# Performance work log

Measured on AMD Instinct MI355X. Metric: run time of the kernel, lower is better.

Reference implementation:

```python
import jax, jax.numpy as jnp
import numpy as np
from jax import lax

B, T_DEC, T_ENC = 32, 400, 300
N_MEL, PRENET, ENC_D = 80, 256, 512
ATT_RNN, DEC_RNN, ATT_D = 512, 512, 128
LOC_F, LOC_K = 32, 31


def setup_inputs() -> dict:
    key = jax.random.key(0)
    ks = jax.random.split(key, 24)

    def w(k, shape):
        return jax.random.normal(k, shape, jnp.float32) / np.float32(np.sqrt(shape[-1]))

    inp = {
        "encoder_out": jax.random.normal(ks[0], (B, T_ENC, ENC_D), jnp.float32),
        "mels": jax.random.normal(ks[1], (B, T_DEC, N_MEL), jnp.float32),
        "lengths": jax.random.randint(ks[2], (B,), 1, T_ENC + 1).astype(jnp.int32),
        # prenet (3 layers, no bias)
        "W_p0": w(ks[3], (PRENET, N_MEL)),
        "W_p1": w(ks[4], (PRENET, PRENET)),
        "W_p2": w(ks[5], (PRENET, PRENET)),
        # attention GRUCell: input = prenet_dim + enc_dim = 768
        "W_ih_a": w(ks[6], (3 * ATT_RNN, PRENET + ENC_D)),
        "W_hh_a": w(ks[7], (3 * ATT_RNN, ATT_RNN)),
        "b_ih_a": jnp.zeros((3 * ATT_RNN,), jnp.float32),
        "b_hh_a": jnp.zeros((3 * ATT_RNN,), jnp.float32),
        # decoder GRUCell: input = attn_rnn + enc_dim = 1024 (what the code actually feeds)
        "W_ih_d": w(ks[8], (3 * DEC_RNN, ATT_RNN + ENC_D)),
        "W_hh_d": w(ks[9], (3 * DEC_RNN, DEC_RNN)),
        "b_ih_d": jnp.zeros((3 * DEC_RNN,), jnp.float32),
        "b_hh_d": jnp.zeros((3 * DEC_RNN,), jnp.float32),
        # location-sensitive attention
        "W_q": w(ks[10], (ATT_D, ATT_RNN)),
        "W_m": w(ks[11], (ATT_D, ENC_D)),
        "K_loc": w(ks[12], (LOC_F, 2, LOC_K)),
        "W_l": w(ks[13], (ATT_D, LOC_F)),
        "v": w(ks[14], (ATT_D,)),
        # output projection + gate
        "W_out": w(ks[15], (N_MEL, DEC_RNN + ENC_D)),
        "b_out": jnp.zeros((N_MEL,), jnp.float32),
        "W_g": w(ks[16], (1, DEC_RNN + ENC_D)),
        "b_g": jnp.zeros((1,), jnp.float32),
    }
    return inp


def _gru_cell(x, h, W_ih, W_hh, b_ih, b_hh):
    gi = x @ W_ih.T + b_ih
    gh = h @ W_hh.T + b_hh
    i_r, i_z, i_n = jnp.split(gi, 3, axis=-1)
    h_r, h_z, h_n = jnp.split(gh, 3, axis=-1)
    r = jax.nn.sigmoid(i_r + h_r)
    z = jax.nn.sigmoid(i_z + h_z)
    n = jnp.tanh(i_n + r * h_n)
    return (1.0 - z) * n + z * h


def _decoder_core(encoder_out, mels, lengths, W_p0, W_p1, W_p2,
                  W_ih_a, W_hh_a, b_ih_a, b_hh_a, W_ih_d, W_hh_d, b_ih_d, b_hh_d,
                  W_q, W_m, K_loc, W_l, v, W_out, b_out, W_g, b_g):
    Bb, T_enc, _ = encoder_out.shape
    T_dec = mels.shape[1]
    pmem = encoder_out @ W_m.T  # [B,T_enc,ATT_D], computed once
    enc_mask = jnp.arange(T_enc)[None, :] < lengths[:, None]  # [B,T_enc]
    # shifted teacher-forcing inputs: zero first frame, then mels[:, :-1]
    dec_inputs = jnp.concatenate(
        [jnp.zeros((Bb, 1, mels.shape[2]), mels.dtype), mels[:, :-1]], axis=1)
    drop_key = jax.random.key(42)
    pad = LOC_K // 2

    def prenet(x, t):
        for i, W in enumerate((W_p0, W_p1, W_p2)):
            x = jax.nn.relu(x @ W.T)
            k = jax.random.fold_in(drop_key, t * 3 + i)
            keep = jax.random.bernoulli(k, 0.5, x.shape)
            x = jnp.where(keep, x * 2.0, 0.0)  # inverted dropout p=0.5 (hardcoded training=True)
        return x

    def step(carry, xs):
        ah, dh, ctx, aw, aw_sum = carry
        frame, t = xs
        x = prenet(frame, t)
        ah = _gru_cell(jnp.concatenate([x, ctx], -1), ah, W_ih_a, W_hh_a, b_ih_a, b_hh_a)
        # location features from current + cumulative attention weights
        awc = jnp.stack([aw, aw_sum], axis=1)  # [B,2,T_enc]
        loc = lax.conv_general_dilated(awc, K_loc, (1,), [(pad, pad)],
                                       dimension_numbers=("NCH", "OIH", "NCH"))
        loc = jnp.swapaxes(loc, 1, 2) @ W_l.T  # [B,T_enc,ATT_D]
        e = jnp.tanh((ah @ W_q.T)[:, None, :] + pmem + loc) @ v  # [B,T_enc]
        e = jnp.where(enc_mask, e, -1e9)
        aw_new = jax.nn.softmax(e, axis=-1)
        ctx = jnp.einsum("bt,btd->bd", aw_new, encoder_out)
        aw_sum = aw_sum + aw_new
        dh = _gru_cell(jnp.concatenate([ah, ctx], -1), dh, W_ih_d, W_hh_d, b_ih_d, b_hh_d)
        dhc = jnp.concatenate([dh, ctx], -1)
        mel = dhc @ W_out.T + b_out  # [B,N_MEL]
        gate = (dhc @ W_g.T + b_g)[:, 0]  # [B]
        return (ah, dh, ctx, aw_new, aw_sum), (mel, gate, aw_new)

    f32 = encoder_out.dtype
    init = (jnp.zeros((Bb, ATT_RNN), f32), jnp.zeros((Bb, DEC_RNN), f32),
            jnp.zeros((Bb, ENC_D), f32), jnp.zeros((Bb, T_enc), f32),
            jnp.zeros((Bb, T_enc), f32))
    frames = jnp.swapaxes(dec_inputs, 0, 1)  # [T_dec,B,N_MEL]
    _, (mels_out, gates, aligns) = lax.scan(jax.checkpoint(step), init,
                                            (frames, jnp.arange(T_dec)))
    mel_outputs = jnp.transpose(mels_out, (1, 2, 0))  # [B,N_MEL,T_dec]
    gate_outputs = jnp.swapaxes(gates, 0, 1)          # [B,T_dec]
    alignments = jnp.swapaxes(aligns, 0, 1)           # [B,T_dec,T_enc]
    return mel_outputs, gate_outputs, alignments


def reference(encoder_out, mels, lengths, W_p0, W_p1, W_p2,
              W_ih_a, W_hh_a, b_ih_a, b_hh_a, W_ih_d, W_hh_d, b_ih_d, b_hh_d,
              W_q, W_m, K_loc, W_l, v, W_out, b_out, W_g, b_g):
    return _decoder_core(encoder_out, mels, lengths, W_p0, W_p1, W_p2,
                         W_ih_a, W_hh_a, b_ih_a, b_hh_a, W_ih_d, W_hh_d, b_ih_d, b_hh_d,
                         W_q, W_m, K_loc, W_l, v, W_out, b_out, W_g, b_g)
```

## Files before the change

### kernel.cpp

```cpp
#include <hip/hip_runtime.h>
#include <cstdint>


static constexpr int TDEC = 400, TENC = 300, NMEL = 80;

__device__ __forceinline__ uint2 threefry2x32(uint32_t k0, uint32_t k1,
                                              uint32_t x0, uint32_t x1) {
  uint32_t k2 = k0 ^ k1 ^ 0x1BD11BDAu;
  x0 += k0; x1 += k1;
#define TFR(r) { x0 += x1; x1 = (x1 << (r)) | (x1 >> (32 - (r))); x1 ^= x0; }
  TFR(13) TFR(15) TFR(26) TFR(6)
  x0 += k1; x1 += k2 + 1u;
  TFR(17) TFR(29) TFR(16) TFR(24)
  x0 += k2; x1 += k0 + 2u;
  TFR(13) TFR(15) TFR(26) TFR(6)
  x0 += k0; x1 += k1 + 3u;
  TFR(17) TFR(29) TFR(16) TFR(24)
  x0 += k1; x1 += k2 + 4u;
  TFR(13) TFR(15) TFR(26) TFR(6)
  x0 += k2; x1 += k0 + 5u;
#undef TFR
  return make_uint2(x0, x1);
}

__device__ __forceinline__ bool keep_mask(uint32_t key0, uint32_t key1, uint32_t idx) {
  uint2 o = threefry2x32(key0, key1, 0u, idx);
  uint32_t bits = o.x ^ o.y;
  float u = __uint_as_float((bits >> 9) | 0x3f800000u) - 1.0f;
  return u < 0.5f;
}

__device__ __forceinline__ float dot4(float4 w, float4 a) {
  return w.x * a.x + w.y * a.y + w.z * a.z + w.w * a.w;
}
__device__ __forceinline__ float nt_load(const float* p) {
  return __builtin_nontemporal_load(p);
}

__device__ __forceinline__ void s_rel(float* p, float v) {
  __hip_atomic_store(p, v, __ATOMIC_RELAXED, __HIP_MEMORY_SCOPE_AGENT);
}
__device__ __forceinline__ float l_rel(const float* p) {
  return __hip_atomic_load(p, __ATOMIC_RELAXED, __HIP_MEMORY_SCOPE_AGENT);
}
__device__ __forceinline__ float4 l4(const float4* p) {
  const unsigned long long* q = (const unsigned long long*)p;
  unsigned long long a = __hip_atomic_load(q, __ATOMIC_RELAXED, __HIP_MEMORY_SCOPE_AGENT);
  unsigned long long b = __hip_atomic_load(q + 1, __ATOMIC_RELAXED, __HIP_MEMORY_SCOPE_AGENT);
  float4 r;
  ((unsigned long long*)&r)[0] = a;
  ((unsigned long long*)&r)[1] = b;
  return r;
}

__device__ __forceinline__ void gsync(int* arrive, int* release, int bno) {
  __syncthreads();
  if (blockIdx.x == 0) {
    if (threadIdx.x > 0)
      while (__hip_atomic_load(&arrive[threadIdx.x * 32], __ATOMIC_RELAXED,
                               __HIP_MEMORY_SCOPE_AGENT) < bno)
        __builtin_amdgcn_s_sleep(16);
    __syncthreads();
    if (threadIdx.x < 8)
      __hip_atomic_store(&release[threadIdx.x * 32], bno, __ATOMIC_RELEASE,
                         __HIP_MEMORY_SCOPE_AGENT);
  } else {
    if (threadIdx.x == 0) {
      __hip_atomic_store(&arrive[blockIdx.x * 32], bno, __ATOMIC_RELEASE,
                         __HIP_MEMORY_SCOPE_AGENT);
      while (__hip_atomic_load(&release[(blockIdx.x & 7) * 32], __ATOMIC_RELAXED,
                               __HIP_MEMORY_SCOPE_AGENT) < bno)
        __builtin_amdgcn_s_sleep(16);
    }
  }
  __syncthreads();
}

template <int K>
__device__ __forceinline__ void prenet_layer(const float* in_lds, float* out_lds,
                                             float* out_g, const float* __restrict__ W,
                                             uint32_t key0, uint32_t key1, int b0) {
  const int tid = threadIdx.x;
  const int cgp = tid & 63, bg = tid >> 6;
  float acc[4][4];
#pragma unroll
  for (int cc = 0; cc < 4; ++cc)
#pragma unroll
    for (int rr = 0; rr < 4; ++rr) acc[cc][rr] = 0.f;
  const float4* W4 = (const float4*)W;
  const float4* in4 = (const float4*)in_lds;
  for (int k4 = 0; k4 < K / 4; ++k4) {
    float4 a[4];
#pragma unroll
    for (int rr = 0; rr < 4; ++rr) a[rr] = in4[(bg * 4 + rr) * (K / 4) + k4];
#pragma unroll
    for (int cc = 0; cc < 4; ++cc) {
      float4 w = W4[(cgp + 64 * cc) * (K / 4) + k4];
#pragma unroll
      for (int rr = 0; rr < 4; ++rr) acc[cc][rr] += dot4(w, a[rr]);
    }
  }
#pragma unroll
  for (int cc = 0; cc < 4; ++cc)
#pragma unroll
    for (int rr = 0; rr < 4; ++rr) {
      int c = cgp + 64 * cc, br = bg * 4 + rr;
      float val = fmaxf(acc[cc][rr], 0.f);
      val = keep_mask(key0, key1, (uint32_t)((b0 + br) * 256 + c)) ? val * 2.f : 0.f;
      if (out_lds) out_lds[br * 256 + c] = val;
      if (out_g) out_g[(b0 + br) * 256 + c] = val;
    }
  __syncthreads();
}

__global__ __launch_bounds__(256) void prenet_kernel(const float* __restrict__ mels,
                                                     const float* __restrict__ Wp0,
                                                     const float* __restrict__ Wp1,
                                                     const float* __restrict__ Wp2,
                                                     float* __restrict__ x_all) {
  __shared__ float bufA[16 * 256];
  __shared__ float bufB[16 * 256];
  const int t = blockIdx.x >> 1, b0 = (blockIdx.x & 1) * 16;
  const int tid = threadIdx.x;
  for (int i = tid; i < 16 * 80; i += 256) {
    int br = i / 80, k = i % 80;
    bufB[br * 80 + k] = (t == 0) ? 0.f : mels[((b0 + br) * TDEC + (t - 1)) * NMEL + k];
  }
  __syncthreads();
  uint2 k0v = threefry2x32(0u, 42u, 0u, (uint32_t)(t * 3 + 0));
  uint2 k1v = threefry2x32(0u, 42u, 0u, (uint32_t)(t * 3 + 1));
  uint2 k2v = threefry2x32(0u, 42u, 0u, (uint32_t)(t * 3 + 2));
  prenet_layer<80>(bufB, bufA, nullptr, Wp0, k0v.x, k0v.y, b0);
  prenet_layer<256>(bufA, bufB, nullptr, Wp1, k1v.x, k1v.y, b0);
  prenet_layer<256>(bufB, nullptr, x_all + t * 8192, Wp2, k2v.x, k2v.y, b0);
}

__global__ __launch_bounds__(256) void pmem_kernel(const float* __restrict__ enc,
                                                   const float* __restrict__ Wm,
                                                   float* __restrict__ pmem) {
  const int b = blockIdx.x / 10, pc = blockIdx.x % 10;
  const int j = threadIdx.x & 127, ph = threadIdx.x >> 7;
  const float4* Wm4 = (const float4*)Wm;
  const float4* enc4 = (const float4*)enc + (size_t)(b * 300 + pc * 30 + ph * 15) * 128;
  float acc[15];
#pragma unroll
  for (int pp = 0; pp < 15; ++pp) acc[pp] = 0.f;
  for (int k4 = 0; k4 < 128; ++k4) {
    float4 w = Wm4[j * 128 + k4];
#pragma unroll
    for (int pp = 0; pp < 15; ++pp) acc[pp] += dot4(w, enc4[pp * 128 + k4]);
  }
#pragma unroll
  for (int pp = 0; pp < 15; ++pp)
    pmem[(size_t)(b * 300 + pc * 30 + ph * 15 + pp) * 128 + j] = acc[pp];
}

struct DP {
  const float *xall, *enc, *pmem;
  const int* lens;
  const float *Wiha, *Whha, *biha, *bhha;
  const float *Wihd, *Whhd, *bihd, *bhhd;
  const float *Wq, *Kloc, *Wl, *vv, *Wout, *bout, *Wg, *bg;
  float *ah, *dh, *ctxM;
  float *e2;
  float *pM, *pS;
  float *V;
  float *awsum2;
  int *arrive, *release, *rM;
  float *omel, *ogate, *oalign;
};

__global__ __launch_bounds__(256, 1) void decoder_kernel(DP P) {
  __shared__ float4 pinW[4608];
  __shared__ float scr[6144];
  __shared__ float2 tapsL[992];
  const int tid = threadIdx.x, blk = blockIdx.x;
  const int er = blk >> 2, eq = blk & 3, pb = eq * 75;

  if (blk < 128) {
    const float4* Wih4 = (const float4*)P.Wiha;
    const float4* Whh4 = (const float4*)P.Whha;
    int idx0 = blk * 4;
    for (int i = tid; i < 2304; i += 256) {
      int g = i / 768, rem = i % 768, r2 = rem / 192, k4 = rem % 192;
      pinW[i] = Wih4[(size_t)(g * 512 + idx0 + r2) * 192 + k4];
    }
    for (int i = tid; i < 1536; i += 256) {
      int g = i / 512, rem = i % 512, r2 = rem / 128, k4 = rem % 128;
      pinW[2304 + i] = Whh4[(size_t)(g * 512 + idx0 + r2) * 128 + k4];
    }
  } else {
    const float4* Wih4 = (const float4*)P.Wihd;
    const float4* Whh4 = (const float4*)P.Whhd;
    int idx0 = (blk - 128) * 4;
    for (int i = tid; i < 3072; i += 256) {
      int g = i / 1024, rem = i % 1024, r2 = rem / 256, k4 = rem % 256;
      pinW[i] = Wih4[(size_t)(g * 512 + idx0 + r2) * 256 + k4];
    }
    for (int i = tid; i < 1536; i += 256) {
      int g = i / 512, rem = i % 512, r2 = rem / 128, k4 = rem % 128;
      pinW[3072 + i] = Whh4[(size_t)(g * 512 + idx0 + r2) * 128 + k4];
    }
  }
  for (int i = tid; i < 992; i += 256) {
    int f = i / 31, k = i % 31;
    tapsL[i] = make_float2(P.Kloc[f * 62 + k], P.Kloc[f * 62 + 31 + k]);
  }
  __syncthreads();

  int bno = 0;
  for (int t = 0; t <= TDEC; ++t) {
    const int p0 = t & 1, p1 = p0 ^ 1;

    {
      const bool isAtt = (blk < 128);
      const bool act = isAtt ? (t < TDEC) : (t >= 1);
      if (act) {
        const int row = tid >> 3, seg = tid & 7;
        const int idx0 = (isAtt ? blk : (blk - 128)) * 4;
        const int K4I = isAtt ? 192 : 256;
        const int SI = K4I / 8, a4n = isAtt ? 64 : 128;
        const float4* WihL = pinW;
        const float4* WhhL = pinW + (isAtt ? 2304 : 3072);
        const float4* A4p = isAtt ? (const float4*)(P.xall + (size_t)t * 8192) : nullptr;
        const float4* Ab = isAtt ? nullptr : (const float4*)(P.ah + p1 * 16384);
        const float4* C4 = (const float4*)(P.ctxM + p1 * 16384);
        const float4* H4 = isAtt ? (const float4*)(P.ah + p1 * 16384)
                                 : (const float4*)(P.dh + p0 * 16384);
        const float* bih = isAtt ? P.biha : P.bihd;
        const float* bhh = isAtt ? P.bhha : P.bhhd;
        const float* hpv = isAtt ? (P.ah + p1 * 16384) : (P.dh + p0 * 16384);
        float* hout = isAtt ? (P.ah + p0 * 16384) : (P.dh + p1 * 16384);

        float acc[24];
#pragma unroll
        for (int g = 0; g < 24; ++g) acc[g] = 0.f;
        for (int sb = 0; sb < SI; sb += 8) {
          float4 av[8];
#pragma unroll
          for (int u = 0; u < 8; ++u) {
            int k4 = (sb + u) * 8 + seg;
            if (k4 < a4n) av[u] = isAtt ? A4p[row * a4n + k4] : l4(&Ab[row * a4n + k4]);
            else av[u] = l4(&C4[row * 128 + (k4 - a4n)]);
          }
#pragma unroll
          for (int u = 0; u < 8; ++u) {
            int k4 = (sb + u) * 8 + seg;
#pragma unroll
            for (int g = 0; g < 3; ++g)
#pragma unroll
              for (int i = 0; i < 4; ++i)
                acc[g * 4 + i] += dot4(WihL[(g * 4 + i) * K4I + k4], av[u]);
          }
        }
        for (int sb = 0; sb < 16; sb += 8) {
          float4 hv[8];
#pragma unroll
          for (int u = 0; u < 8; ++u) {
            int k4 = (sb + u) * 8 + seg;
            hv[u] = l4(&H4[row * 128 + k4]);
          }
#pragma unroll
          for (int u = 0; u < 8; ++u) {
            int k4 = (sb + u) * 8 + seg;
#pragma unroll
            for (int g = 0; g < 3; ++g)
#pragma unroll
              for (int i = 0; i < 4; ++i)
                acc[12 + g * 4 + i] += dot4(WhhL[(g * 4 + i) * 128 + k4], hv[u]);
          }
        }
#pragma unroll
        for (int g = 0; g < 24; ++g) scr[(g * 32 + row) * 8 + seg] = acc[g];
        __syncthreads();
        if (tid < 128) {
          int i = tid >> 5, r = tid & 31;
          float gi[3], gh[3];
#pragma unroll
          for (int g = 0; g < 3; ++g) {
            float si = 0.f, sh = 0.f;
#pragma unroll
            for (int s = 0; s < 8; ++s) {
              si += scr[((g * 4 + i) * 32 + r) * 8 + s];
              sh += scr[((12 + g * 4 + i) * 32 + r) * 8 + s];
            }
            gi[g] = si + bih[g * 512 + idx0 + i];
            gh[g] = sh + bhh[g * 512 + idx0 + i];
          }
          float rr = 1.f / (1.f + expf(-(gi[0] + gh[0])));
          float zz = 1.f / (1.f + expf(-(gi[1] + gh[1])));
          float nn = tanhf(gi[2] + rr * gh[2]);
          float hp = l_rel(&hpv[r * 512 + idx0 + i]);
          s_rel(&hout[r * 512 + idx0 + i], (1.f - zz) * nn + zz * hp);
        }
      }
    }
    gsync(P.arrive, P.release, ++bno);

    if (blk < 128) {
      float* awW = scr;
      float* asW = scr + 105;
      float* convl = scr + 216;
      float* qp = scr + 2688;
      float* qb = scr + 2944;
      float* el = scr + 3072;
      float* eex = scr + 3152;
      float* ahS = scr + 3232;

      if (t < TDEC) {
        float v0s = l_rel(&P.ah[p0 * 16384 + er * 512 + tid]);
        float v1s = l_rel(&P.ah[p0 * 16384 + er * 512 + 256 + tid]);
        ahS[tid] = v0s;
        ahS[256 + tid] = v1s;
      }

      if (t >= 1) {
        float pMv[4], pSv[4];
#pragma unroll
        for (int j = 0; j < 4; ++j) pMv[j] = l_rel(&P.pM[p1 * 128 + er * 4 + j]);
#pragma unroll
        for (int j = 0; j < 4; ++j) pSv[j] = l_rel(&P.pS[p1 * 128 + er * 4 + j]);
        float M = fmaxf(fmaxf(pMv[0], pMv[1]), fmaxf(pMv[2], pMv[3]));
        float Z = 0.f;
#pragma unroll
        for (int j = 0; j < 4; ++j) Z += pSv[j] * expf(pMv[j] - M);
        float inv = 1.f / Z;
        for (int i = tid; i < 105; i += 256) {
          int p = pb - 15 + i;
          float a = 0.f, s = 0.f;
          if (p >= 0 && p < TENC) {
            float ev = l_rel(&P.e2[p1 * 9728 + er * 304 + p]);
            float sv = l_rel(&P.awsum2[p1 * 9600 + er * 300 + p]);
            a = expf(ev - M) * inv;
            s = sv + a;
          }
          awW[i] = a;
          asW[i] = s;
          if (p >= pb && p < pb + 75) {
            s_rel(&P.awsum2[p0 * 9600 + er * 300 + p], s);
            P.oalign[((size_t)(er * 400 + (t - 1))) * 300 + p] = a;
          }
        }
      } else {
        for (int i = tid; i < 105; i += 256) { awW[i] = 0.f; asW[i] = 0.f; }
      }
      __syncthreads();

      if (t < TDEC) {
        {
          int f = tid & 31, pl0 = tid >> 5;
          for (int pl = pl0; pl < 75; pl += 8) {
            float a = 0.f;
#pragma unroll
            for (int k = 0; k < 31; ++k) {
              float2 tv = tapsL[f * 31 + k];
              a += awW[pl + k] * tv.x + asW[pl + k] * tv.y;
            }
            convl[f * 77 + pl] = a;
          }
        }
        {
          int j = tid & 127, kh = tid >> 7;
          const float4* Wq4 = (const float4*)P.Wq;
          const float4* a4 = (const float4*)ahS;
          float acc = 0.f;
          for (int k4 = kh * 64; k4 < kh * 64 + 64; ++k4)
            acc += dot4(Wq4[j * 128 + k4], a4[k4]);
          qp[j * 2 + kh] = acc;
        }
        __syncthreads();
        if (tid < 128) qb[tid] = qp[tid * 2] + qp[tid * 2 + 1];
        __syncthreads();
        {
          int w = tid >> 6, lane = tid & 63;
          float wl0[32], wl1[32];
#pragma unroll
          for (int f = 0; f < 32; ++f) {
            wl0[f] = P.Wl[lane * 32 + f];
            wl1[f] = P.Wl[(lane + 64) * 32 + f];
          }
          float v0 = P.vv[lane], v1 = P.vv[lane + 64];
          float q0 = qb[lane], q1 = qb[64 + lane];
          int len = P.lens[er];
          for (int pl = w; pl < 75; pl += 4) {
            int p = pb + pl;
            float a0 = 0.f, a1 = 0.f;
#pragma unroll
            for (int f = 0; f < 32; ++f) {
              float c = convl[f * 77 + pl];
              a0 += c * wl0[f];
              a1 += c * wl1[f];
            }
            float e0 = tanhf(q0 + P.pmem[((size_t)er * 300 + p) * 128 + lane] + a0) * v0;
            float e1 = tanhf(q1 + P.pmem[((size_t)er * 300 + p) * 128 + 64 + lane] + a1) * v1;
            float es = e0 + e1;
#pragma unroll
            for (int off = 32; off > 0; off >>= 1) es += __shfl_xor(es, off, 64);
            if (lane == 0) {
              float ev = (p < len) ? es : -1e9f;
              s_rel(&P.e2[p0 * 9728 + er * 304 + p], ev);
              el[pl] = ev;
            }
          }
        }
        __syncthreads();
        if (tid < 64) {
          int lane = tid;
          float m = -3.4e38f;
          for (int i = lane; i < 75; i += 64) m = fmaxf(m, el[i]);
#pragma unroll
          for (int off = 32; off > 0; off >>= 1) m = fmaxf(m, __shfl_xor(m, off, 64));
          float s = 0.f;
          for (int i = lane; i < 75; i += 64) {
            float x = expf(el[i] - m);
            eex[i] = x;
            s += x;
          }
#pragma unroll
          for (int off = 32; off > 0; off >>= 1) s += __shfl_xor(s, off, 64);
          if (lane == 0) {
            s_rel(&P.pM[p0 * 128 + er * 4 + eq], m);
            s_rel(&P.pS[p0 * 128 + er * 4 + eq], s);
          }
        }
        __syncthreads();
        {
          float* Vw = P.V + (size_t)p0 * 65536 + (size_t)(er * 4 + eq) * 512;
#pragma unroll
          for (int cc = 0; cc < 2; ++cc) {
            int c = tid + cc * 256;
            float acc = 0.f;
            const float* eb = P.enc + ((size_t)(er * 300 + pb)) * 512 + c;
            for (int po = 0; po < 75; ++po) acc += eex[po] * nt_load(eb + (size_t)po * 512);
            s_rel(&Vw[c], acc);
          }
        }
        __syncthreads();
        if (tid == 0)
          __hip_atomic_store(&P.rM[(er * 4 + eq) * 32], t + 1, __ATOMIC_RELEASE,
                             __HIP_MEMORY_SCOPE_AGENT);
        if (eq == 0) {
          if (tid < 3)
            while (__hip_atomic_load(&P.rM[(er * 4 + 1 + tid) * 32], __ATOMIC_RELAXED,
                                     __HIP_MEMORY_SCOPE_AGENT) < t + 1)
              __builtin_amdgcn_s_sleep(8);
          __syncthreads();
          float pMv[4], pSv[4];
#pragma unroll
          for (int j = 0; j < 4; ++j) pMv[j] = l_rel(&P.pM[p0 * 128 + er * 4 + j]);
#pragma unroll
          for (int j = 0; j < 4; ++j) pSv[j] = l_rel(&P.pS[p0 * 128 + er * 4 + j]);
          float M = fmaxf(fmaxf(pMv[0], pMv[1]), fmaxf(pMv[2], pMv[3]));
          float Z = 0.f, wq[4];
#pragma unroll
          for (int j = 0; j < 4; ++j) {
            wq[j] = expf(pMv[j] - M);
            Z += pSv[j] * wq[j];
          }
          float invZ = 1.f / Z;
          const float* Vb = P.V + (size_t)p0 * 65536 + (size_t)(er * 4) * 512;
#pragma unroll
          for (int cc = 0; cc < 2; ++cc) {
            int c = tid + cc * 256;
            float vv4[4];
#pragma unroll
            for (int j = 0; j < 4; ++j) vv4[j] = l_rel(&Vb[j * 512 + c]);
            float acc = vv4[0] * wq[0] + vv4[1] * wq[1] + vv4[2] * wq[2] + vv4[3] * wq[3];
            s_rel(&P.ctxM[p0 * 16384 + er * 512 + c], acc * invZ);
          }
        }
      }
    } else if (blk < 160) {
      if (t >= 1) {
        const int r = blk - 128;
        float* dhcx = scr;
        float* opl = scr + 1024;
        for (int i = tid; i < 512; i += 256) {
          float d0 = l_rel(&P.dh[p1 * 16384 + r * 512 + i]);
          float c0 = l_rel(&P.ctxM[p1 * 16384 + r * 512 + i]);
          dhcx[i] = d0;
          dhcx[512 + i] = c0;
        }
        __syncthreads();
        if (tid < 162) {
          int m = tid >> 1, h = tid & 1;
          const float4* W4 = (m < 80) ? ((const float4*)P.Wout + (size_t)m * 256)
                                      : (const float4*)P.Wg;
          const float4* x4 = (const float4*)dhcx;
          float a = 0.f;
          for (int k4 = h * 128; k4 < h * 128 + 128; ++k4) a += dot4(W4[k4], x4[k4]);
          opl[tid] = a;
        }
        __syncthreads();
        if (tid < 81) {
          float sum = opl[tid * 2] + opl[tid * 2 + 1];
          if (tid < 80) P.omel[(size_t)(r * 80 + tid) * 400 + (t - 1)] = sum + P.bout[tid];
          else P.ogate[r * 400 + (t - 1)] = sum + P.bg[0];
        }
      }
    }
    gsync(P.arrive, P.release, ++bno);
  }
}

extern "C" void kernel_launch(void* const* d_in, const int* in_sizes, int n_in,
                              void* d_out, int out_size, void* d_ws, size_t ws_size,
                              hipStream_t stream) {
  const float* enc = (const float*)d_in[0];
  const float* mels = (const float*)d_in[1];
  const int* lens = (const int*)d_in[2];

  float* ws = (float*)d_ws;
  float* x_all = ws;
  float* pmem = x_all + 3276800;
  float* ah = pmem + 1228800;
  float* dh = ah + 32768;
  float* ctxM = dh + 32768;
  float* e2 = ctxM + 32768;
  float* pM = e2 + 19456;
  float* pS = pM + 256;
  float* V = pS + 256;
  float* awsum2 = V + 131072;
  int* arrive = (int*)(awsum2 + 19200);
  int* release = arrive + 8192;
  int* rM = release + 256;

  (void)hipMemsetAsync(ah, 0, (3 * 32768) * sizeof(float), stream);
  (void)hipMemsetAsync(awsum2, 0, 19200 * sizeof(float), stream);
  (void)hipMemsetAsync(arrive, 0, (8192 + 256 + 4096) * sizeof(int), stream);

  prenet_kernel<<<800, 256, 0, stream>>>(mels, (const float*)d_in[3],
                                         (const float*)d_in[4], (const float*)d_in[5],
                                         x_all);
  pmem_kernel<<<320, 256, 0, stream>>>(enc, (const float*)d_in[15], pmem);

  float* omel = (float*)d_out;
  float* ogate = omel + 32 * 80 * 400;
  float* oalign = ogate + 32 * 400;

  DP P;
  P.xall = x_all; P.enc = enc; P.pmem = pmem; P.lens = lens;
  P.Wiha = (const float*)d_in[6]; P.Whha = (const float*)d_in[7];
  P.biha = (const float*)d_in[8]; P.bhha = (const float*)d_in[9];
  P.Wihd = (const float*)d_in[10]; P.Whhd = (const float*)d_in[11];
  P.bihd = (const float*)d_in[12]; P.bhhd = (const float*)d_in[13];
  P.Wq = (const float*)d_in[14]; P.Kloc = (const float*)d_in[16];
  P.Wl = (const float*)d_in[17]; P.vv = (const float*)d_in[18];
  P.Wout = (const float*)d_in[19]; P.bout = (const float*)d_in[20];
  P.Wg = (const float*)d_in[21]; P.bg = (const float*)d_in[22];
  P.ah = ah; P.dh = dh; P.ctxM = ctxM; P.e2 = e2; P.pM = pM; P.pS = pS; P.V = V;
  P.awsum2 = awsum2;
  P.arrive = arrive; P.release = release; P.rM = rM;
  P.omel = omel; P.ogate = ogate; P.oalign = oalign;

  decoder_kernel<<<256, 256, 0, stream>>>(P);
}
```

Before: 48.70 ms.

## Decouple attention and decoder block groups with ring buffers and separate barriers

Splits the persistent kernel into two independently synchronized groups: attention blocks run their own per-step barriers and publish step progress, while decoder GRU and output blocks lag behind via an 8-deep ring buffer of attention hidden state and context. This replaces the single grid-wide barrier per step with group-local barriers, so the decoder chain can overlap with later attention steps. It also caches the processed-memory slice in LDS instead of reading it from global memory each step. The trade-offs are more workspace, flow-control spin waits, and extra LDS use.

```diff
diff --git a/kernel.cpp b/kernel.cpp
--- a/kernel.cpp
+++ b/kernel.cpp
@@ -3,6 +3,7 @@
 
 
 static constexpr int TDEC = 400, TENC = 300, NMEL = 80;
+static constexpr int RING = 8;
 
 __device__ __forceinline__ uint2 threefry2x32(uint32_t k0, uint32_t k1,
                                               uint32_t x0, uint32_t x1) {
@@ -43,6 +44,9 @@
 __device__ __forceinline__ float l_rel(const float* p) {
   return __hip_atomic_load(p, __ATOMIC_RELAXED, __HIP_MEMORY_SCOPE_AGENT);
 }
+__device__ __forceinline__ int li_rel(const int* p) {
+  return __hip_atomic_load(p, __ATOMIC_RELAXED, __HIP_MEMORY_SCOPE_AGENT);
+}
 __device__ __forceinline__ float4 l4(const float4* p) {
   const unsigned long long* q = (const unsigned long long*)p;
   unsigned long long a = __hip_atomic_load(q, __ATOMIC_RELAXED, __HIP_MEMORY_SCOPE_AGENT);
@@ -53,24 +57,24 @@
   return r;
 }
 
-__device__ __forceinline__ void gsync(int* arrive, int* release, int bno) {
+__device__ __forceinline__ void gsyncN(int* arrive, int* release, int id, int bno) {
   __syncthreads();
-  if (blockIdx.x == 0) {
-    if (threadIdx.x > 0)
+  if (id == 0) {
+    if (threadIdx.x > 0 && threadIdx.x < 128)
       while (__hip_atomic_load(&arrive[threadIdx.x * 32], __ATOMIC_RELAXED,
                                __HIP_MEMORY_SCOPE_AGENT) < bno)
-        __builtin_amdgcn_s_sleep(16);
+        __builtin_amdgcn_s_sleep(8);
     __syncthreads();
     if (threadIdx.x < 8)
       __hip_atomic_store(&release[threadIdx.x * 32], bno, __ATOMIC_RELEASE,
                          __HIP_MEMORY_SCOPE_AGENT);
   } else {
     if (threadIdx.x == 0) {
-      __hip_atomic_store(&arrive[blockIdx.x * 32], bno, __ATOMIC_RELEASE,
+      __hip_atomic_store(&arrive[id * 32], bno, __ATOMIC_RELEASE,
                          __HIP_MEMORY_SCOPE_AGENT);
-      while (__hip_atomic_load(&release[(blockIdx.x & 7) * 32], __ATOMIC_RELAXED,
+      while (__hip_atomic_load(&release[(id & 7) * 32], __ATOMIC_RELAXED,
                                __HIP_MEMORY_SCOPE_AGENT) < bno)
-        __builtin_amdgcn_s_sleep(16);
+        __builtin_amdgcn_s_sleep(8);
     }
   }
   __syncthreads();
@@ -161,12 +165,13 @@
   const float *Wiha, *Whha, *biha, *bhha;
   const float *Wihd, *Whhd, *bihd, *bhhd;
   const float *Wq, *Kloc, *Wl, *vv, *Wout, *bout, *Wg, *bg;
-  float *ah, *dh, *ctxM;
+  float *ah, *ctxM;
+  float *dh;
   float *e2;
   float *pM, *pS;
   float *V;
   float *awsum2;
-  int *arrive, *release, *rM;
+  int *arrA, *relA, *arrD, *relD, *rM, *attT, *decT;
   float *omel, *ogate, *oalign;
 };
 
@@ -174,74 +179,60 @@
   __shared__ float4 pinW[4608];
   __shared__ float scr[6144];
   __shared__ float2 tapsL[992];
+  __shared__ float pmemL[9600];
   const int tid = threadIdx.x, blk = blockIdx.x;
-  const int er = blk >> 2, eq = blk & 3, pb = eq * 75;
 
   if (blk < 128) {
-    const float4* Wih4 = (const float4*)P.Wiha;
-    const float4* Whh4 = (const float4*)P.Whha;
-    int idx0 = blk * 4;
-    for (int i = tid; i < 2304; i += 256) {
-      int g = i / 768, rem = i % 768, r2 = rem / 192, k4 = rem % 192;
-      pinW[i] = Wih4[(size_t)(g * 512 + idx0 + r2) * 192 + k4];
+    const int er = blk >> 2, eq = blk & 3, pb = eq * 75;
+    const int idx0 = blk * 4;
+    {
+      const float4* Wih4 = (const float4*)P.Wiha;
+      const float4* Whh4 = (const float4*)P.Whha;
+      for (int i = tid; i < 2304; i += 256) {
+        int g = i / 768, rem = i % 768, r2 = rem / 192, k4 = rem % 192;
+        pinW[i] = Wih4[(size_t)(g * 512 + idx0 + r2) * 192 + k4];
+      }
+      for (int i = tid; i < 1536; i += 256) {
+        int g = i / 512, rem = i % 512, r2 = rem / 128, k4 = rem % 128;
+        pinW[2304 + i] = Whh4[(size_t)(g * 512 + idx0 + r2) * 128 + k4];
+      }
+      for (int i = tid; i < 992; i += 256) {
+        int f = i / 31, k = i % 31;
+        tapsL[i] = make_float2(P.Kloc[f * 62 + k], P.Kloc[f * 62 + 31 + k]);
+      }
+      for (int i = tid; i < 9600; i += 256) {
+        int pl = i >> 7, c = i & 127;
+        pmemL[pl * 128 + c] = P.pmem[((size_t)(er * 300 + pb + pl)) * 128 + c];
+      }
     }
-    for (int i = tid; i < 1536; i += 256) {
-      int g = i / 512, rem = i % 512, r2 = rem / 128, k4 = rem % 128;
-      pinW[2304 + i] = Whh4[(size_t)(g * 512 + idx0 + r2) * 128 + k4];
-    }
-  } else {
-    const float4* Wih4 = (const float4*)P.Wihd;
-    const float4* Whh4 = (const float4*)P.Whhd;
-    int idx0 = (blk - 128) * 4;
-    for (int i = tid; i < 3072; i += 256) {
-      int g = i / 1024, rem = i % 1024, r2 = rem / 256, k4 = rem % 256;
-      pinW[i] = Wih4[(size_t)(g * 512 + idx0 + r2) * 256 + k4];
-    }
-    for (int i = tid; i < 1536; i += 256) {
-      int g = i / 512, rem = i % 512, r2 = rem / 128, k4 = rem % 128;
-      pinW[3072 + i] = Whh4[(size_t)(g * 512 + idx0 + r2) * 128 + k4];
-    }
-  }
-  for (int i = tid; i < 992; i += 256) {
-    int f = i / 31, k = i % 31;
-    tapsL[i] = make_float2(P.Kloc[f * 62 + k], P.Kloc[f * 62 + 31 + k]);
-  }
-  __syncthreads();
-
-  int bno = 0;
-  for (int t = 0; t <= TDEC; ++t) {
-    const int p0 = t & 1, p1 = p0 ^ 1;
-
-    {
-      const bool isAtt = (blk < 128);
-      const bool act = isAtt ? (t < TDEC) : (t >= 1);
-      if (act) {
+    __syncthreads();
+
+    int bno = 0;
+    for (int t = 0; t <= TDEC; ++t) {
+      const int p0 = t & 1, p1 = p0 ^ 1;
+      const int sc = t & (RING - 1), sp = (t - 1) & (RING - 1);
+      float* ahC = P.ah + sc * 16384;
+      const float* ahP = P.ah + sp * 16384;
+      const float* ctxP = P.ctxM + sp * 16384;
+
+      if (tid == 0)
+        while (li_rel(P.decT) < t - 7) __builtin_amdgcn_s_sleep(16);
+      __syncthreads();
+
+      if (t < TDEC) {
         const int row = tid >> 3, seg = tid & 7;
-        const int idx0 = (isAtt ? blk : (blk - 128)) * 4;
-        const int K4I = isAtt ? 192 : 256;
-        const int SI = K4I / 8, a4n = isAtt ? 64 : 128;
-        const float4* WihL = pinW;
-        const float4* WhhL = pinW + (isAtt ? 2304 : 3072);
-        const float4* A4p = isAtt ? (const float4*)(P.xall + (size_t)t * 8192) : nullptr;
-        const float4* Ab = isAtt ? nullptr : (const float4*)(P.ah + p1 * 16384);
-        const float4* C4 = (const float4*)(P.ctxM + p1 * 16384);
-        const float4* H4 = isAtt ? (const float4*)(P.ah + p1 * 16384)
-                                 : (const float4*)(P.dh + p0 * 16384);
-        const float* bih = isAtt ? P.biha : P.bihd;
-        const float* bhh = isAtt ? P.bhha : P.bhhd;
-        const float* hpv = isAtt ? (P.ah + p1 * 16384) : (P.dh + p0 * 16384);
-        float* hout = isAtt ? (P.ah + p0 * 16384) : (P.dh + p1 * 16384);
-
+        const float4* A4p = (const float4*)(P.xall + (size_t)t * 8192);
+        const float4* C4 = (const float4*)ctxP;
+        const float4* H4 = (const float4*)ahP;
         float acc[24];
 #pragma unroll
         for (int g = 0; g < 24; ++g) acc[g] = 0.f;
-        for (int sb = 0; sb < SI; sb += 8) {
+        for (int sb = 0; sb < 24; sb += 8) {
           float4 av[8];
 #pragma unroll
           for (int u = 0; u < 8; ++u) {
             int k4 = (sb + u) * 8 + seg;
-            if (k4 < a4n) av[u] = isAtt ? A4p[row * a4n + k4] : l4(&Ab[row * a4n + k4]);
-            else av[u] = l4(&C4[row * 128 + (k4 - a4n)]);
+            av[u] = (k4 < 64) ? A4p[row * 64 + k4] : l4(&C4[row * 128 + (k4 - 64)]);
           }
 #pragma unroll
           for (int u = 0; u < 8; ++u) {
@@ -250,7 +241,7 @@
             for (int g = 0; g < 3; ++g)
 #pragma unroll
               for (int i = 0; i < 4; ++i)
-                acc[g * 4 + i] += dot4(WihL[(g * 4 + i) * K4I + k4], av[u]);
+                acc[g * 4 + i] += dot4(pinW[(g * 4 + i) * 192 + k4], av[u]);
           }
         }
         for (int sb = 0; sb < 16; sb += 8) {
@@ -267,7 +258,7 @@
             for (int g = 0; g < 3; ++g)
 #pragma unroll
               for (int i = 0; i < 4; ++i)
-                acc[12 + g * 4 + i] += dot4(WhhL[(g * 4 + i) * 128 + k4], hv[u]);
+                acc[12 + g * 4 + i] += dot4(pinW[2304 + (g * 4 + i) * 128 + k4], hv[u]);
           }
         }
 #pragma unroll
@@ -284,206 +275,311 @@
               si += scr[((g * 4 + i) * 32 + r) * 8 + s];
               sh += scr[((12 + g * 4 + i) * 32 + r) * 8 + s];
             }
-            gi[g] = si + bih[g * 512 + idx0 + i];
-            gh[g] = sh + bhh[g * 512 + idx0 + i];
+            gi[g] = si + P.biha[g * 512 + idx0 + i];
+            gh[g] = sh + P.bhha[g * 512 + idx0 + i];
           }
           float rr = 1.f / (1.f + expf(-(gi[0] + gh[0])));
           float zz = 1.f / (1.f + expf(-(gi[1] + gh[1])));
           float nn = tanhf(gi[2] + rr * gh[2]);
-          float hp = l_rel(&hpv[r * 512 + idx0 + i]);
-          s_rel(&hout[r * 512 + idx0 + i], (1.f - zz) * nn + zz * hp);
-        }
-      }
+          float hp = l_rel(&ahP[r * 512 + idx0 + i]);
+          s_rel(&ahC[r * 512 + idx0 + i], (1.f - zz) * nn + zz * hp);
+        }
+      }
+      gsyncN(P.arrA, P.relA, blk, ++bno);
+
+      {
+        float* awW = scr;
+        float* asW = scr + 105;
+        float* convl = scr + 216;
+        float* qp = scr + 2688;
+        float* qb = scr + 2944;
+        float* el = scr + 3072;
+        float* eex = scr + 3152;
+        float* ahS = scr + 3232;
+
+        if (t < TDEC) {
+          float v0s = l_rel(&ahC[er * 512 + tid]);
+          float v1s = l_rel(&ahC[er * 512 + 256 + tid]);
+          ahS[tid] = v0s;
+          ahS[256 + tid] = v1s;
+        }
+        if (t >= 1) {
+          float pMv[4], pSv[4];
+#pragma unroll
+          for (int j = 0; j < 4; ++j) pMv[j] = l_rel(&P.pM[p1 * 128 + er * 4 + j]);
+#pragma unroll
+          for (int j = 0; j < 4; ++j) pSv[j] = l_rel(&P.pS[p1 * 128 + er * 4 + j]);
+          float M = fmaxf(fmaxf(pMv[0], pMv[1]), fmaxf(pMv[2], pMv[3]));
+          float Z = 0.f;
+#pragma unroll
+          for (int j = 0; j < 4; ++j) Z += pSv[j] * expf(pMv[j] - M);
+          float inv = 1.f / Z;
+          for (int i = tid; i < 105; i += 256) {
+            int p = pb - 15 + i;
+            float a = 0.f, s = 0.f;
+            if (p >= 0 && p < TENC) {
+              float ev = l_rel(&P.e2[p1 * 9728 + er * 304 + p]);
+              float sv = l_rel(&P.awsum2[p1 * 9600 + er * 300 + p]);
+              a = expf(ev - M) * inv;
+              s = sv + a;
+            }
+            awW[i] = a;
+            asW[i] = s;
+            if (p >= pb && p < pb + 75) {
+              s_rel(&P.awsum2[p0 * 9600 + er * 300 + p], s);
+              P.oalign[((size_t)(er * 400 + (t - 1))) * 300 + p] = a;
+            }
+          }
+        } else {
+          for (int i = tid; i < 105; i += 256) { awW[i] = 0.f; asW[i] = 0.f; }
+        }
+        __syncthreads();
+
+        if (t < TDEC) {
+          {
+            int f = tid & 31, pl0 = tid >> 5;
+            for (int pl = pl0; pl < 75; pl += 8) {
+              float a = 0.f;
+#pragma unroll
+              for (int k = 0; k < 31; ++k) {
+                float2 tv = tapsL[f * 31 + k];
+                a += awW[pl + k] * tv.x + asW[pl + k] * tv.y;
+              }
+              convl[f * 77 + pl] = a;
+            }
+          }
+          {
+            int j = tid & 127, kh = tid >> 7;
+            const float4* Wq4 = (const float4*)P.Wq;
+            const float4* a4 = (const float4*)ahS;
+            float acc = 0.f;
+            for (int k4 = kh * 64; k4 < kh * 64 + 64; ++k4)
+              acc += dot4(Wq4[j * 128 + k4], a4[k4]);
+            qp[j * 2 + kh] = acc;
+          }
+          __syncthreads();
+          if (tid < 128) qb[tid] = qp[tid * 2] + qp[tid * 2 + 1];
+          __syncthreads();
+          {
+            int w = tid >> 6, lane = tid & 63;
+            float wl0[32], wl1[32];
+#pragma unroll
+            for (int f = 0; f < 32; ++f) {
+              wl0[f] = P.Wl[lane * 32 + f];
+              wl1[f] = P.Wl[(lane + 64) * 32 + f];
+            }
+            float v0 = P.vv[lane], v1 = P.vv[lane + 64];
+            float q0 = qb[lane], q1 = qb[64 + lane];
+            int len = P.lens[er];
+            for (int pl = w; pl < 75; pl += 4) {
+              int p = pb + pl;
+              float a0 = 0.f, a1 = 0.f;
+#pragma unroll
+              for (int f = 0; f < 32; ++f) {
+                float c = convl[f * 77 + pl];
+                a0 += c * wl0[f];
+                a1 += c * wl1[f];
+              }
+              float e0 = tanhf(q0 + pmemL[pl * 128 + lane] + a0) * v0;
+              float e1 = tanhf(q1 + pmemL[pl * 128 + 64 + lane] + a1) * v1;
+              float es = e0 + e1;
+#pragma unroll
+              for (int off = 32; off > 0; off >>= 1) es += __shfl_xor(es, off, 64);
+              if (lane == 0) {
+                float ev = (p < len) ? es : -1e9f;
+                s_rel(&P.e2[p0 * 9728 + er * 304 + p], ev);
+                el[pl] = ev;
+              }
+            }
+          }
+          __syncthreads();
+          if (tid < 64) {
+            int lane = tid;
+            float m = -3.4e38f;
+            for (int i = lane; i < 75; i += 64) m = fmaxf(m, el[i]);
+#pragma unroll
+            for (int off = 32; off > 0; off >>= 1) m = fmaxf(m, __shfl_xor(m, off, 64));
+            float s = 0.f;
+            for (int i = lane; i < 75; i += 64) {
+              float x = expf(el[i] - m);
+              eex[i] = x;
+              s += x;
+            }
+#pragma unroll
+            for (int off = 32; off > 0; off >>= 1) s += __shfl_xor(s, off, 64);
+            if (lane == 0) {
+              s_rel(&P.pM[p0 * 128 + er * 4 + eq], m);
+              s_rel(&P.pS[p0 * 128 + er * 4 + eq], s);
+            }
+          }
+          __syncthreads();
+          {
+            float* Vw = P.V + (size_t)p0 * 65536 + (size_t)(er * 4 + eq) * 512;
+#pragma unroll
+            for (int cc = 0; cc < 2; ++cc) {
+              int c = tid + cc * 256;
+              float acc = 0.f;
+              const float* eb = P.enc + ((size_t)(er * 300 + pb)) * 512 + c;
+              for (int po = 0; po < 75; ++po) acc += eex[po] * nt_load(eb + (size_t)po * 512);
+              s_rel(&Vw[c], acc);
+            }
+          }
+          __syncthreads();
+          if (tid == 0)
+            __hip_atomic_store(&P.rM[(er * 4 + eq) * 32], t + 1, __ATOMIC_RELEASE,
+                               __HIP_MEMORY_SCOPE_AGENT);
+          if (eq == 0) {
+            if (tid < 3)
+              while (__hip_atomic_load(&P.rM[(er * 4 + 1 + tid) * 32], __ATOMIC_RELAXED,
+                                       __HIP_MEMORY_SCOPE_AGENT) < t + 1)
+                __builtin_amdgcn_s_sleep(4);
+            __syncthreads();
+            float pMv[4], pSv[4];
+#pragma unroll
+            for (int j = 0; j < 4; ++j) pMv[j] = l_rel(&P.pM[p0 * 128 + er * 4 + j]);
+#pragma unroll
+            for (int j = 0; j < 4; ++j) pSv[j] = l_rel(&P.pS[p0 * 128 + er * 4 + j]);
+            float M = fmaxf(fmaxf(pMv[0], pMv[1]), fmaxf(pMv[2], pMv[3]));
+            float Z = 0.f, wq[4];
+#pragma unroll
+            for (int j = 0; j < 4; ++j) {
+              wq[j] = expf(pMv[j] - M);
+              Z += pSv[j] * wq[j];
+            }
+            float invZ = 1.f / Z;
+            const float* Vb = P.V + (size_t)p0 * 65536 + (size_t)(er * 4) * 512;
+            float* ctxC = P.ctxM + sc * 16384;
+#pragma unroll
+            for (int cc = 0; cc < 2; ++cc) {
+              int c = tid + cc * 256;
+              float vv4[4];
+#pragma unroll
+              for (int j = 0; j < 4; ++j) vv4[j] = l_rel(&Vb[j * 512 + c]);
+              float acc = vv4[0] * wq[0] + vv4[1] * wq[1] + vv4[2] * wq[2] + vv4[3] * wq[3];
+              s_rel(&ctxC[er * 512 + c], acc * invZ);
+            }
+          }
+        }
+      }
+      gsyncN(P.arrA, P.relA, blk, ++bno);
+      if (blk == 0 && tid == 0)
+        __hip_atomic_store(P.attT, t + 1, __ATOMIC_RELEASE, __HIP_MEMORY_SCOPE_AGENT);
     }
-    gsync(P.arrive, P.release, ++bno);
-
-    if (blk < 128) {
-      float* awW = scr;
-      float* asW = scr + 105;
-      float* convl = scr + 216;
-      float* qp = scr + 2688;
-      float* qb = scr + 2944;
-      float* el = scr + 3072;
-      float* eex = scr + 3152;
-      float* ahS = scr + 3232;
-
-      if (t < TDEC) {
-        float v0s = l_rel(&P.ah[p0 * 16384 + er * 512 + tid]);
-        float v1s = l_rel(&P.ah[p0 * 16384 + er * 512 + 256 + tid]);
-        ahS[tid] = v0s;
-        ahS[256 + tid] = v1s;
-      }
-
-      if (t >= 1) {
-        float pMv[4], pSv[4];
-#pragma unroll
-        for (int j = 0; j < 4; ++j) pMv[j] = l_rel(&P.pM[p1 * 128 + er * 4 + j]);
-#pragma unroll
-        for (int j = 0; j < 4; ++j) pSv[j] = l_rel(&P.pS[p1 * 128 + er * 4 + j]);
-        float M = fmaxf(fmaxf(pMv[0], pMv[1]), fmaxf(pMv[2], pMv[3]));
-        float Z = 0.f;
-#pragma unroll
-        for (int j = 0; j < 4; ++j) Z += pSv[j] * expf(pMv[j] - M);
-        float inv = 1.f / Z;
-        for (int i = tid; i < 105; i += 256) {
-          int p = pb - 15 + i;
-          float a = 0.f, s = 0.f;
-          if (p >= 0 && p < TENC) {
-            float ev = l_rel(&P.e2[p1 * 9728 + er * 304 + p]);
-            float sv = l_rel(&P.awsum2[p1 * 9600 + er * 300 + p]);
-            a = expf(ev - M) * inv;
-            s = sv + a;
-          }
-          awW[i] = a;
-          asW[i] = s;
-          if (p >= pb && p < pb + 75) {
-            s_rel(&P.awsum2[p0 * 9600 + er * 300 + p], s);
-            P.oalign[((size_t)(er * 400 + (t - 1))) * 300 + p] = a;
-          }
-        }
-      } else {
-        for (int i = tid; i < 105; i += 256) { awW[i] = 0.f; asW[i] = 0.f; }
-      }
+  } else {
+    const int dblk = blk - 128;
+    const int idx0 = dblk * 4;
+    const int r_op = dblk >> 2, mq = dblk & 3;
+    const int m0 = (mq == 0) ? 0 : 21 + 20 * (mq - 1);
+    const int mcnt = (mq == 0) ? 21 : 20;
+    {
+      const float4* Wih4 = (const float4*)P.Wihd;
+      const float4* Whh4 = (const float4*)P.Whhd;
+      for (int i = tid; i < 3072; i += 256) {
+        int g = i / 1024, rem = i % 1024, r2 = rem / 256, k4 = rem % 256;
+        pinW[i] = Wih4[(size_t)(g * 512 + idx0 + r2) * 256 + k4];
+      }
+      for (int i = tid; i < 1536; i += 256) {
+        int g = i / 512, rem = i % 512, r2 = rem / 128, k4 = rem % 128;
+        pinW[3072 + i] = Whh4[(size_t)(g * 512 + idx0 + r2) * 128 + k4];
+      }
+    }
+    __syncthreads();
+
+    int bno = 0;
+    for (int t = 0; t < TDEC; ++t) {
+      const int p0 = t & 1, p1 = p0 ^ 1;
+      const int sc = t & (RING - 1);
+      const float* ahC = P.ah + sc * 16384;
+      const float* ctxC = P.ctxM + sc * 16384;
+      float* dhW = P.dh + p0 * 16384;
+      const float* dhP = P.dh + p1 * 16384;
+
+      if (tid == 0)
+        while (li_rel(P.attT) < t + 1) __builtin_amdgcn_s_sleep(16);
       __syncthreads();
 
-      if (t < TDEC) {
-        {
-          int f = tid & 31, pl0 = tid >> 5;
-          for (int pl = pl0; pl < 75; pl += 8) {
-            float a = 0.f;
-#pragma unroll
-            for (int k = 0; k < 31; ++k) {
-              float2 tv = tapsL[f * 31 + k];
-              a += awW[pl + k] * tv.x + asW[pl + k] * tv.y;
-            }
-            convl[f * 77 + pl] = a;
-          }
-        }
-        {
-          int j = tid & 127, kh = tid >> 7;
-          const float4* Wq4 = (const float4*)P.Wq;
-          const float4* a4 = (const float4*)ahS;
-          float acc = 0.f;
-          for (int k4 = kh * 64; k4 < kh * 64 + 64; ++k4)
-            acc += dot4(Wq4[j * 128 + k4], a4[k4]);
-          qp[j * 2 + kh] = acc;
-        }
+      {
+        const int row = tid >> 3, seg = tid & 7;
+        const float4* A4 = (const float4*)ahC;
+        const float4* C4 = (const float4*)ctxC;
+        const float4* H4 = (const float4*)dhP;
+        float acc[24];
+#pragma unroll
+        for (int g = 0; g < 24; ++g) acc[g] = 0.f;
+        for (int sb = 0; sb < 32; sb += 8) {
+          float4 av[8];
+#pragma unroll
+          for (int u = 0; u < 8; ++u) {
+            int k4 = (sb + u) * 8 + seg;
+            av[u] = (k4 < 128) ? l4(&A4[row * 128 + k4]) : l4(&C4[row * 128 + (k4 - 128)]);
+          }
+#pragma unroll
+          for (int u = 0; u < 8; ++u) {
+            int k4 = (sb + u) * 8 + seg;
+#pragma unroll
+            for (int g = 0; g < 3; ++g)
+#pragma unroll
+              for (int i = 0; i < 4; ++i)
+                acc[g * 4 + i] += dot4(pinW[(g * 4 + i) * 256 + k4], av[u]);
+          }
+        }
+        for (int sb = 0; sb < 16; sb += 8) {
+          float4 hv[8];
+#pragma unroll
+          for (int u = 0; u < 8; ++u) {
+            int k4 = (sb + u) * 8 + seg;
+            hv[u] = l4(&H4[row * 128 + k4]);
+          }
+#pragma unroll
+          for (int u = 0; u < 8; ++u) {
+            int k4 = (sb + u) * 8 + seg;
+#pragma unroll
+            for (int g = 0; g < 3; ++g)
+#pragma unroll
+              for (int i = 0; i < 4; ++i)
+                acc[12 + g * 4 + i] += dot4(pinW[3072 + (g * 4 + i) * 128 + k4], hv[u]);
+          }
+        }
+#pragma unroll
+        for (int g = 0; g < 24; ++g) scr[(g * 32 + row) * 8 + seg] = acc[g];
         __syncthreads();
-        if (tid < 128) qb[tid] = qp[tid * 2] + qp[tid * 2 + 1];
-        __syncthreads();
-        {
-          int w = tid >> 6, lane = tid & 63;
-          float wl0[32], wl1[32];
-#pragma unroll
-          for (int f = 0; f < 32; ++f) {
-            wl0[f] = P.Wl[lane * 32 + f];
-            wl1[f] = P.Wl[(lane + 64) * 32 + f];
-          }
-          float v0 = P.vv[lane], v1 = P.vv[lane + 64];
-          float q0 = qb[lane], q1 = qb[64 + lane];
-          int len = P.lens[er];
-          for (int pl = w; pl < 75; pl += 4) {
-            int p = pb + pl;
-            float a0 = 0.f, a1 = 0.f;
-#pragma unroll
-            for (int f = 0; f < 32; ++f) {
-              float c = convl[f * 77 + pl];
-              a0 += c * wl0[f];
-              a1 += c * wl1[f];
-            }
-            float e0 = tanhf(q0 + P.pmem[((size_t)er * 300 + p) * 128 + lane] + a0) * v0;
-            float e1 = tanhf(q1 + P.pmem[((size_t)er * 300 + p) * 128 + 64 + lane] + a1) * v1;
-            float es = e0 + e1;
-#pragma unroll
-            for (int off = 32; off > 0; off >>= 1) es += __shfl_xor(es, off, 64);
-            if (lane == 0) {
-              float ev = (p < len) ? es : -1e9f;
-              s_rel(&P.e2[p0 * 9728 + er * 304 + p], ev);
-              el[pl] = ev;
-            }
-          }
-        }
-        __syncthreads();
-        if (tid < 64) {
-          int lane = tid;
-          float m = -3.4e38f;
-          for (int i = lane; i < 75; i += 64) m = fmaxf(m, el[i]);
-#pragma unroll
-          for (int off = 32; off > 0; off >>= 1) m = fmaxf(m, __shfl_xor(m, off, 64));
-          float s = 0.f;
-          for (int i = lane; i < 75; i += 64) {
-            float x = expf(el[i] - m);
-            eex[i] = x;
-            s += x;
-          }
-#pragma unroll
-          for (int off = 32; off > 0; off >>= 1) s += __shfl_xor(s, off, 64);
-          if (lane == 0) {
-            s_rel(&P.pM[p0 * 128 + er * 4 + eq], m);
-            s_rel(&P.pS[p0 * 128 + er * 4 + eq], s);
-          }
-        }
-        __syncthreads();
-        {
-          float* Vw = P.V + (size_t)p0 * 65536 + (size_t)(er * 4 + eq) * 512;
-#pragma unroll
-          for (int cc = 0; cc < 2; ++cc) {
-            int c = tid + cc * 256;
-            float acc = 0.f;
-            const float* eb = P.enc + ((size_t)(er * 300 + pb)) * 512 + c;
-            for (int po = 0; po < 75; ++po) acc += eex[po] * nt_load(eb + (size_t)po * 512);
-            s_rel(&Vw[c], acc);
-          }
-        }
-        __syncthreads();
-        if (tid == 0)
-          __hip_atomic_store(&P.rM[(er * 4 + eq) * 32], t + 1, __ATOMIC_RELEASE,
-                             __HIP_MEMORY_SCOPE_AGENT);
-        if (eq == 0) {
-          if (tid < 3)
-            while (__hip_atomic_load(&P.rM[(er * 4 + 1 + tid) * 32], __ATOMIC_RELAXED,
-                                     __HIP_MEMORY_SCOPE_AGENT) < t + 1)
-              __builtin_amdgcn_s_sleep(8);
-          __syncthreads();
-          float pMv[4], pSv[4];
-#pragma unroll
-          for (int j = 0; j < 4; ++j) pMv[j] = l_rel(&P.pM[p0 * 128 + er * 4 + j]);
-#pragma unroll
-          for (int j = 0; j < 4; ++j) pSv[j] = l_rel(&P.pS[p0 * 128 + er * 4 + j]);
-          float M = fmaxf(fmaxf(pMv[0], pMv[1]), fmaxf(pMv[2], pMv[3]));
-          float Z = 0.f, wq[4];
-#pragma unroll
-          for (int j = 0; j < 4; ++j) {
-            wq[j] = expf(pMv[j] - M);
-            Z += pSv[j] * wq[j];
-          }
-          float invZ = 1.f / Z;
-          const float* Vb = P.V + (size_t)p0 * 65536 + (size_t)(er * 4) * 512;
-#pragma unroll
-          for (int cc = 0; cc < 2; ++cc) {
-            int c = tid + cc * 256;
-            float vv4[4];
-#pragma unroll
-            for (int j = 0; j < 4; ++j) vv4[j] = l_rel(&Vb[j * 512 + c]);
-            float acc = vv4[0] * wq[0] + vv4[1] * wq[1] + vv4[2] * wq[2] + vv4[3] * wq[3];
-            s_rel(&P.ctxM[p0 * 16384 + er * 512 + c], acc * invZ);
-          }
-        }
-      }
-    } else if (blk < 160) {
-      if (t >= 1) {
-        const int r = blk - 128;
+        if (tid < 128) {
+          int i = tid >> 5, r = tid & 31;
+          float gi[3], gh[3];
+#pragma unroll
+          for (int g = 0; g < 3; ++g) {
+            float si = 0.f, sh = 0.f;
+#pragma unroll
+            for (int s = 0; s < 8; ++s) {
+              si += scr[((g * 4 + i) * 32 + r) * 8 + s];
+              sh += scr[((12 + g * 4 + i) * 32 + r) * 8 + s];
+            }
+            gi[g] = si + P.bihd[g * 512 + idx0 + i];
+            gh[g] = sh + P.bhhd[g * 512 + idx0 + i];
+          }
+          float rr = 1.f / (1.f + expf(-(gi[0] + gh[0])));
+          float zz = 1.f / (1.f + expf(-(gi[1] + gh[1])));
+          float nn = tanhf(gi[2] + rr * gh[2]);
+          float hp = l_rel(&dhP[r * 512 + idx0 + i]);
+          s_rel(&dhW[r * 512 + idx0 + i], (1.f - zz) * nn + zz * hp);
+        }
+      }
+      gsyncN(P.arrD, P.relD, dblk, ++bno);
+      if (dblk == 0 && tid == 0)
+        __hip_atomic_store(P.decT, t, __ATOMIC_RELEASE, __HIP_MEMORY_SCOPE_AGENT);
+
+      {
         float* dhcx = scr;
         float* opl = scr + 1024;
         for (int i = tid; i < 512; i += 256) {
-          float d0 = l_rel(&P.dh[p1 * 16384 + r * 512 + i]);
-          float c0 = l_rel(&P.ctxM[p1 * 16384 + r * 512 + i]);
+          float d0 = l_rel(&dhW[r_op * 512 + i]);
+          float c0 = l_rel(&ctxC[r_op * 512 + i]);
           dhcx[i] = d0;
           dhcx[512 + i] = c0;
         }
         __syncthreads();
-        if (tid < 162) {
-          int m = tid >> 1, h = tid & 1;
+        if (tid < 2 * mcnt) {
+          int m = m0 + (tid >> 1), h = tid & 1;
           const float4* W4 = (m < 80) ? ((const float4*)P.Wout + (size_t)m * 256)
                                       : (const float4*)P.Wg;
           const float4* x4 = (const float4*)dhcx;
@@ -492,14 +588,15 @@
           opl[tid] = a;
         }
         __syncthreads();
-        if (tid < 81) {
+        if (tid < mcnt) {
+          int m = m0 + tid;
           float sum = opl[tid * 2] + opl[tid * 2 + 1];
-          if (tid < 80) P.omel[(size_t)(r * 80 + tid) * 400 + (t - 1)] = sum + P.bout[tid];
-          else P.ogate[r * 400 + (t - 1)] = sum + P.bg[0];
-        }
+          if (m < 80) P.omel[(size_t)(r_op * 80 + m) * 400 + t] = sum + P.bout[m];
+          else P.ogate[r_op * 400 + t] = sum + P.bg[0];
+        }
+        __syncthreads();
       }
     }
-    gsync(P.arrive, P.release, ++bno);
   }
 }
 
@@ -514,20 +611,25 @@
   float* x_all = ws;
   float* pmem = x_all + 3276800;
   float* ah = pmem + 1228800;
-  float* dh = ah + 32768;
-  float* ctxM = dh + 32768;
-  float* e2 = ctxM + 32768;
+  float* ctxM = ah + 131072;
+  float* dh = ctxM + 131072;
+  float* e2 = dh + 32768;
   float* pM = e2 + 19456;
   float* pS = pM + 256;
   float* V = pS + 256;
   float* awsum2 = V + 131072;
-  int* arrive = (int*)(awsum2 + 19200);
-  int* release = arrive + 8192;
-  int* rM = release + 256;
-
-  (void)hipMemsetAsync(ah, 0, (3 * 32768) * sizeof(float), stream);
+  int* arrA = (int*)(awsum2 + 19200);
+  int* relA = arrA + 4096;
+  int* arrD = relA + 256;
+  int* relD = arrD + 4096;
+  int* rM = relD + 256;
+  int* attT = rM + 4096;
+  int* decT = attT + 32;
+
+  (void)hipMemsetAsync(ah, 0, (131072 + 131072 + 32768) * sizeof(float), stream);
   (void)hipMemsetAsync(awsum2, 0, 19200 * sizeof(float), stream);
-  (void)hipMemsetAsync(arrive, 0, (8192 + 256 + 4096) * sizeof(int), stream);
+  (void)hipMemsetAsync(arrA, 0, (4096 + 256 + 4096 + 256 + 4096 + 32 + 32) * sizeof(int),
+                       stream);
 
   prenet_kernel<<<800, 256, 0, stream>>>(mels, (const float*)d_in[3],
                                          (const float*)d_in[4], (const float*)d_in[5],
@@ -548,9 +650,10 @@
   P.Wl = (const float*)d_in[17]; P.vv = (const float*)d_in[18];
   P.Wout = (const float*)d_in[19]; P.bout = (const float*)d_in[20];
   P.Wg = (const float*)d_in[21]; P.bg = (const float*)d_in[22];
-  P.ah = ah; P.dh = dh; P.ctxM = ctxM; P.e2 = e2; P.pM = pM; P.pS = pS; P.V = V;
+  P.ah = ah; P.ctxM = ctxM; P.dh = dh; P.e2 = e2; P.pM = pM; P.pS = pS; P.V = V;
   P.awsum2 = awsum2;
-  P.arrive = arrive; P.release = release; P.rM = rM;
+  P.arrA = arrA; P.relA = relA; P.arrD = arrD; P.relD = relD; P.rM = rM;
+  P.attT = attT; P.decT = decT;
   P.omel = omel; P.ogate = ogate; P.oalign = oalign;
 
   decoder_kernel<<<256, 256, 0, stream>>>(P);
```

Result: faster. 45.37 ms (-6.8%).
